# Kernel tuning notes

Hardware: AMD Instinct MI355X
Metric: run time of the kernel (lower is better)

Reference implementation:

```python
import jax, jax.numpy as jnp
import numpy as np
from jax import lax

N, CIN, P, CH, COUT = 1024, 3, 14, 256, 3
DN = ('NCHW', 'OIHW', 'NCHW')


def _conv(x, w, b, pad=1):
    y = lax.conv_general_dilated(x, w, (1, 1), [(pad, pad), (pad, pad)], dimension_numbers=DN)
    return y + b[None, :, None, None]


def _conv_transpose(x, w_t, b):
    # PyTorch ConvTranspose2d(k=3, stride=2, padding=1, output_padding=1):
    # equivalent to conv with lhs_dilation=2, padding (k-1-p, k-1-p+op) = (1, 2),
    # kernel with in/out swapped and spatially flipped. w_t: [in, out, 3, 3]
    w = jnp.flip(jnp.transpose(w_t, (1, 0, 2, 3)), axis=(2, 3))  # [out, in, 3, 3]
    y = lax.conv_general_dilated(x, w, (1, 1), [(1, 2), (1, 2)], lhs_dilation=(2, 2),
                                 dimension_numbers=DN)
    return y + b[None, :, None, None]


def setup_inputs() -> dict:
    key = jax.random.key(0)
    ks = jax.random.split(key, 16)
    s3 = lambda cin: 1.0 / np.sqrt(cin * 9)
    inp = {"x": jax.random.normal(ks[0], (N, CIN, P, P), dtype=jnp.float32)}
    inp["w1"] = jax.random.normal(ks[1], (CH, CIN, 3, 3), jnp.float32) * s3(CIN)
    inp["b1"] = jnp.zeros((CH,), jnp.float32)
    inp["w2"] = jax.random.normal(ks[2], (CH, CH, 3, 3), jnp.float32) * s3(CH)
    inp["b2"] = jnp.zeros((CH,), jnp.float32)
    inp["w3"] = jax.random.normal(ks[3], (CH, CH, 3, 3), jnp.float32) * s3(CH)
    inp["b3"] = jnp.zeros((CH,), jnp.float32)
    inp["w4"] = jax.random.normal(ks[4], (CH, CH, 3, 3), jnp.float32) * s3(CH)
    inp["b4"] = jnp.zeros((CH,), jnp.float32)
    inp["wt"] = jax.random.normal(ks[5], (CH, CH, 3, 3), jnp.float32) * s3(CH)  # [in, out, kh, kw]
    inp["bt"] = jnp.zeros((CH,), jnp.float32)
    inp["w5"] = jax.random.normal(ks[6], (COUT, CH, 1, 1), jnp.float32) * (1.0 / np.sqrt(CH))
    inp["b5"] = jnp.zeros((COUT,), jnp.float32)
    return inp


def reference(x, w1, b1, w2, b2, w3, b3, w4, b4, wt, bt, w5, b5):
    h = jax.nn.relu(_conv(x, w1, b1))
    h = jax.nn.relu(_conv(h, w2, b2))
    h = jax.nn.relu(_conv(h, w3, b3))
    h = jax.nn.relu(_conv(h, w4, b4))
    h = jax.nn.relu(_conv_transpose(h, wt, bt))  # [N, 256, 2P, 2P]
    h = _conv(h, w5, b5, pad=0)                   # 1x1 conv -> [N, 3, 2P, 2P]
    return jax.nn.sigmoid(h)
```

## Files before the change

### kernel.cpp

```cpp
#include <hip/hip_runtime.h>
#include <hip/hip_fp16.h>

typedef _Float16 half8 __attribute__((ext_vector_type(8)));
typedef _Float16 half4 __attribute__((ext_vector_type(4)));
typedef float floatx4 __attribute__((ext_vector_type(4)));

#define PLANE 65536
#define PK_ELEMS 589824

__global__ void repack_kernel(const float* __restrict__ w2, const float* __restrict__ w3,
                              const float* __restrict__ w4, const float* __restrict__ wt,
                              _Float16* __restrict__ pk) {
    int t = blockIdx.x * 256 + threadIdx.x;
    int l = t & 63;
    int idx = t >> 6;
    int nt = idx & 15; idx >>= 4;
    int ks = idx & 7;  idx >>= 3;
    int tap = idx % 9;
    int layer = idx / 9;
    int co = nt * 16 + (l & 15);
    int ci0 = ks * 32 + (l >> 4) * 8;
    const float* w = (layer == 0) ? w2 : (layer == 1) ? w3 : (layer == 2) ? w4 : wt;
    _Float16* dst = pk + (size_t)layer * PK_ELEMS + (((size_t)(tap * 8 + ks) * 16 + nt) * 64 + l) * 8;
    if (layer < 3) {
        for (int j = 0; j < 8; ++j)
            dst[j] = (_Float16)w[(co * 256 + (ci0 + j)) * 9 + tap];
    } else {
        int ky = tap / 3, kx = tap % 3;
        for (int j = 0; j < 8; ++j)
            dst[j] = (_Float16)w[((ci0 + j) * 256 + co) * 9 + (2 - ky) * 3 + (2 - kx)];
    }
}

__global__ __launch_bounds__(1024, 4) void conv1_kernel(const float* __restrict__ x,
                                                        const float* __restrict__ w1,
                                                        const float* __restrict__ b1,
                                                        _Float16* __restrict__ act) {
    __shared__ float inl[3][16][16];
    __shared__ float lw[256 * 27];
    __shared__ float lb1[256];
    int n = blockIdx.x, tid = threadIdx.x;
    if (tid < 768) ((float*)inl)[tid] = 0.f;
    __syncthreads();
    for (int i = tid; i < 3 * 196; i += 1024) {
        int ci = i / 196, r = i % 196, y = r / 14, xx = r % 14;
        inl[ci][y + 1][xx + 1] = x[(size_t)n * 588 + i];
    }
    for (int i = tid; i < 256 * 27; i += 1024) lw[i] = w1[i];
    if (tid < 256) lb1[tid] = b1[tid];
    __syncthreads();
    int p = tid >> 2, q = tid & 3;
    int py = p >> 4, px = p & 15;
    _Float16* ga = act + (size_t)n * PLANE + p * 256;
    int sw = (p & 7) << 3;
    if (py == 0 || py == 15 || px == 0 || px == 15) {
        for (int ci = 0; ci < 64; ++ci) { int co = q + ci * 4; ga[co ^ sw] = (_Float16)0.f; }
    } else {
        float vin[27];
        #pragma unroll
        for (int ci = 0; ci < 3; ++ci)
            #pragma unroll
            for (int ky = 0; ky < 3; ++ky)
                #pragma unroll
                for (int kx = 0; kx < 3; ++kx)
                    vin[ci * 9 + ky * 3 + kx] = inl[ci][py - 1 + ky][px - 1 + kx];
        for (int ci = 0; ci < 64; ++ci) {
            int co = q + ci * 4;
            float acc = lb1[co];
            const float* wp = &lw[co * 27];
            #pragma unroll
            for (int k = 0; k < 27; ++k) acc += vin[k] * wp[k];
            ga[co ^ sw] = (_Float16)fmaxf(acc, 0.f);
        }
    }
}


#define INIT_ACC(BIASPTR)                                                        \
    {                                                                            \
        _Pragma("unroll")                                                        \
        for (int ni = 0; ni < 4; ++ni) {                                         \
            floatx4 bv;                                                          \
            _Pragma("unroll")                                                    \
            for (int reg = 0; reg < 4; ++reg)                                    \
                bv[reg] = (BIASPTR)[(cg * 4 + ni) * 16 + kg * 4 + reg];          \
            _Pragma("unroll")                                                    \
            for (int i = 0; i < 7; ++i) acc[i][ni] = bv;                         \
        }                                                                        \
    }

#define BURST4(AF, BF)                                                           \
    {                                                                            \
        _Pragma("unroll")                                                        \
        for (int j = 0; j < 4; ++j) {                                            \
            acc[j][0] = __builtin_amdgcn_mfma_f32_16x16x32_f16(AF[0], BF[j], acc[j][0], 0, 0, 0); \
            acc[j][1] = __builtin_amdgcn_mfma_f32_16x16x32_f16(AF[1], BF[j], acc[j][1], 0, 0, 0); \
            acc[j][2] = __builtin_amdgcn_mfma_f32_16x16x32_f16(AF[2], BF[j], acc[j][2], 0, 0, 0); \
            acc[j][3] = __builtin_amdgcn_mfma_f32_16x16x32_f16(AF[3], BF[j], acc[j][3], 0, 0, 0); \
        }                                                                        \
    }

#define BURST3(AF, BF)                                                           \
    {                                                                            \
        _Pragma("unroll")                                                        \
        for (int j = 0; j < 3; ++j) {                                            \
            acc[4 + j][0] = __builtin_amdgcn_mfma_f32_16x16x32_f16(AF[0], BF[j], acc[4 + j][0], 0, 0, 0); \
            acc[4 + j][1] = __builtin_amdgcn_mfma_f32_16x16x32_f16(AF[1], BF[j], acc[4 + j][1], 0, 0, 0); \
            acc[4 + j][2] = __builtin_amdgcn_mfma_f32_16x16x32_f16(AF[2], BF[j], acc[4 + j][2], 0, 0, 0); \
            acc[4 + j][3] = __builtin_amdgcn_mfma_f32_16x16x32_f16(AF[3], BF[j], acc[4 + j][3], 0, 0, 0); \
        }                                                                        \
    }

#define LOAD_B4(BF, KS)                                                          \
    {                                                                            \
        int kk_ = ((KS) * 4 + kg) << 3;                                          \
        _Pragma("unroll")                                                        \
        for (int j = 0; j < 4; ++j)                                              \
            BF[j] = *(const half8*)(plane + poff_[j] + (kk_ ^ swj_[j]));         \
    }

#define LOAD_B3(BF, KS)                                                          \
    {                                                                            \
        int kk_ = ((KS) * 4 + kg) << 3;                                          \
        _Pragma("unroll")                                                        \
        for (int j = 0; j < 3; ++j)                                              \
            BF[j] = *(const half8*)(plane + poff_[4 + j] + (kk_ ^ swj_[4 + j])); \
    }

#define LOAD_A(AF, KS)                                                           \
    {                                                                            \
        _Pragma("unroll")                                                        \
        for (int ni = 0; ni < 4; ++ni)                                           \
            AF[ni] = *(const half8*)(pkt_ + (((KS) * 16 + cg * 4 + ni) * 64 + lane) * 8); \
    }

#define ACCUM_TAP(PKT, DOFF)                                                     \
    {                                                                            \
        const _Float16* pkt_ = (PKT);                                            \
        int poff_[7], swj_[7];                                                   \
        _Pragma("unroll")                                                        \
        for (int j = 0; j < 7; ++j) {                                            \
            poff_[j] = (pp[j] + (DOFF)) * 256;                                   \
            swj_[j] = (poff_[j] >> 5) & 56;                                      \
        }                                                                        \
        half8 aP[4], aN[4], bA[4], bB[3];                                        \
        LOAD_A(aP, 0)                                                            \
        LOAD_B4(bA, 0)                                                           \
        _Pragma("clang loop unroll(disable)")                                    \
        for (int ks2 = 0; ks2 < 4; ++ks2) {                                      \
            int e = ks2 * 2, o = e + 1;                                          \
            LOAD_B3(bB, e)                                                       \
            LOAD_A(aN, o)                                                        \
            BURST4(aP, bA)                                                       \
            LOAD_B4(bA, o)                                                       \
            BURST3(aP, bB)                                                       \
            LOAD_B3(bB, o)                                                       \
            if (ks2 < 3) LOAD_A(aP, e + 2)                                       \
            BURST4(aN, bA)                                                       \
            if (ks2 < 3) LOAD_B4(bA, e + 2)                                      \
            BURST3(aN, bB)                                                       \
        }                                                                        \
    }

#define EPILOGUE(RY, RX)                                                         \
    {                                                                            \
        _Pragma("unroll")                                                        \
        for (int i = 0; i < 7; ++i) {                                            \
            float s0 = 0.f, s1 = 0.f, s2 = 0.f;                                  \
            _Pragma("unroll")                                                    \
            for (int ni = 0; ni < 4; ++ni) {                                     \
                int co0 = (cg * 4 + ni) * 16 + kg * 4;                           \
                _Pragma("unroll")                                                \
                for (int reg = 0; reg < 4; ++reg) {                              \
                    float v = fmaxf(acc[i][ni][reg], 0.f);                       \
                    s0 += v * w5l[co0 + reg];                                    \
                    s1 += v * w5l[256 + co0 + reg];                              \
                    s2 += v * w5l[512 + co0 + reg];                              \
                }                                                                \
            }                                                                    \
            s0 += __shfl_xor(s0, 16, 64); s0 += __shfl_xor(s0, 32, 64);          \
            s1 += __shfl_xor(s1, 16, 64); s1 += __shfl_xor(s1, 32, 64);          \
            s2 += __shfl_xor(s2, 16, 64); s2 += __shfl_xor(s2, 32, 64);          \
            if (lane < 14) {                                                     \
                int pt_ = pg + 2 * i;                                            \
                int pix = (2 * pt_ + (RY)) * 28 + 2 * lane + (RX);               \
                atomicAdd(&o3[pix * 3 + 0], s0);                                 \
                atomicAdd(&o3[pix * 3 + 1], s1);                                 \
                atomicAdd(&o3[pix * 3 + 2], s2);                                 \
            }                                                                    \
        }                                                                        \
    }

__global__ __launch_bounds__(512, 2) void fused_kernel(const _Float16* __restrict__ act,
                                                       const _Float16* __restrict__ pk,
                                                       const float* __restrict__ b2,
                                                       const float* __restrict__ b3,
                                                       const float* __restrict__ b4,
                                                       const float* __restrict__ bt,
                                                       const float* __restrict__ w5,
                                                       const float* __restrict__ b5,
                                                       float* __restrict__ out) {
    __shared__ _Float16 plane[PLANE];
    __shared__ float o3[2352];
    __shared__ float w5l[768];
    int n = blockIdx.x, tid = threadIdx.x;
    const _Float16* ga = act + (size_t)n * PLANE;
    #pragma unroll
    for (int i = 0; i < 16; ++i)
        *(uint4*)(plane + (i * 512 + tid) * 8) = *(const uint4*)(ga + (i * 512 + tid) * 8);
    for (int i = tid; i < 2352; i += 512) o3[i] = b5[i % 3];
    for (int i = tid; i < 768; i += 512) w5l[i] = w5[i];

    int lane = tid & 63;
    int wid = __builtin_amdgcn_readfirstlane(tid >> 6);
    int cg = wid >> 1, pg = wid & 1;
    int col = lane & 15, kg = lane >> 4;

    int pp[7];
    {
        int xc = (col < 14) ? col : 13;
        #pragma unroll
        for (int i = 0; i < 7; ++i) pp[i] = (pg + 2 * i + 1) * 16 + xc + 1;
    }
    bool colok = (col < 14);
    __syncthreads();

    floatx4 acc[7][4];

    for (int L = 0; L < 3; ++L) {
        const _Float16* pkL = pk + (size_t)L * PK_ELEMS;
        const float* bias = (L == 0) ? b2 : (L == 1) ? b3 : b4;
        INIT_ACC(bias)
        for (int tap = 0; tap < 9; ++tap) {
            int doff = (tap / 3) * 16 + (tap % 3) - 17;
            ACCUM_TAP(pkL + (size_t)tap * 65536, doff)
        }
        __syncthreads();
        #pragma unroll
        for (int i = 0; i < 7; ++i) {
            int ppix = pp[i];
            int sw = (ppix & 7) << 3;
            if (colok) {
                #pragma unroll
                for (int ni = 0; ni < 4; ++ni) {
                    int co0 = (cg * 4 + ni) * 16 + kg * 4;
                    half4 h;
                    #pragma unroll
                    for (int reg = 0; reg < 4; ++reg) h[reg] = (_Float16)fmaxf(acc[i][ni][reg], 0.f);
                    *(half4*)(plane + ppix * 256 + (co0 ^ sw)) = h;
                }
            }
        }
        __syncthreads();
    }

    const _Float16* pkT = pk + (size_t)3 * PK_ELEMS;
    INIT_ACC(bt)
    ACCUM_TAP(pkT + 4 * 65536, 0)
    EPILOGUE(0, 0)
    INIT_ACC(bt)
    ACCUM_TAP(pkT + 3 * 65536, 0)
    ACCUM_TAP(pkT + 5 * 65536, 1)
    EPILOGUE(0, 1)
    INIT_ACC(bt)
    ACCUM_TAP(pkT + 1 * 65536, 0)
    ACCUM_TAP(pkT + 7 * 65536, 16)
    EPILOGUE(1, 0)
    INIT_ACC(bt)
    ACCUM_TAP(pkT + 0 * 65536, 0)
    ACCUM_TAP(pkT + 2 * 65536, 1)
    ACCUM_TAP(pkT + 6 * 65536, 16)
    ACCUM_TAP(pkT + 8 * 65536, 17)
    EPILOGUE(1, 1)

    __syncthreads();
    size_t ob = (size_t)n * 2352;
    for (int i = tid; i < 2352; i += 512) {
        int pix = i / 3, c = i % 3;
        float v = o3[i];
        out[ob + (size_t)c * 784 + pix] = 1.f / (1.f + __expf(-v));
    }
}

extern "C" void kernel_launch(void* const* d_in, const int* in_sizes, int n_in,
                              void* d_out, int out_size, void* d_ws, size_t ws_size,
                              hipStream_t stream) {
    const float* x  = (const float*)d_in[0];
    const float* w1 = (const float*)d_in[1];
    const float* b1 = (const float*)d_in[2];
    const float* w2 = (const float*)d_in[3];
    const float* b2 = (const float*)d_in[4];
    const float* w3 = (const float*)d_in[5];
    const float* b3 = (const float*)d_in[6];
    const float* w4 = (const float*)d_in[7];
    const float* b4 = (const float*)d_in[8];
    const float* wt = (const float*)d_in[9];
    const float* bt = (const float*)d_in[10];
    const float* w5 = (const float*)d_in[11];
    const float* b5 = (const float*)d_in[12];

    size_t need = ((size_t)1024 * PLANE + 4 * (size_t)PK_ELEMS) * sizeof(_Float16);
    if (ws_size < need) return;

    _Float16* act = (_Float16*)d_ws;
    _Float16* pk  = act + (size_t)1024 * PLANE;

    repack_kernel<<<1152, 256, 0, stream>>>(w2, w3, w4, wt, pk);
    conv1_kernel<<<1024, 1024, 0, stream>>>(x, w1, b1, act);
    fused_kernel<<<1024, 512, 0, stream>>>(act, pk, b2, b3, b4, bt, w5, b5, (float*)d_out);
}
```

Before: 889.8 us.

## Split fused conv work across 12 waves with 3 row groups and guard-padded LDS plane

Raises the fused kernel from 8 to 12 waves per block (768 threads), splitting rows into 3 groups so each wave holds 5 row tiles instead of 7. This cuts accumulator registers per wave and adds wave-level parallelism. Column mapping changes to use lanes 1..14 with zero guard regions around the LDS plane, so halo reads fall into zeroed memory. The cost is more redundant MFMA work on padding rows and columns, plus higher LDS usage per block.

```diff
diff --git a/kernel.cpp b/kernel.cpp
--- a/kernel.cpp
+++ b/kernel.cpp
@@ -7,6 +7,7 @@
 
 #define PLANE 65536
 #define PK_ELEMS 589824
+#define GUARD 4096
 
 __global__ void repack_kernel(const float* __restrict__ w2, const float* __restrict__ w3,
                               const float* __restrict__ w4, const float* __restrict__ wt,
@@ -85,14 +86,14 @@
             for (int reg = 0; reg < 4; ++reg)                                    \
                 bv[reg] = (BIASPTR)[(cg * 4 + ni) * 16 + kg * 4 + reg];          \
             _Pragma("unroll")                                                    \
-            for (int i = 0; i < 7; ++i) acc[i][ni] = bv;                         \
-        }                                                                        \
-    }
-
-#define BURST4(AF, BF)                                                           \
-    {                                                                            \
-        _Pragma("unroll")                                                        \
-        for (int j = 0; j < 4; ++j) {                                            \
+            for (int i = 0; i < 5; ++i) acc[i][ni] = bv;                         \
+        }                                                                        \
+    }
+
+#define BURST3(AF, BF)                                                           \
+    {                                                                            \
+        _Pragma("unroll")                                                        \
+        for (int j = 0; j < 3; ++j) {                                            \
             acc[j][0] = __builtin_amdgcn_mfma_f32_16x16x32_f16(AF[0], BF[j], acc[j][0], 0, 0, 0); \
             acc[j][1] = __builtin_amdgcn_mfma_f32_16x16x32_f16(AF[1], BF[j], acc[j][1], 0, 0, 0); \
             acc[j][2] = __builtin_amdgcn_mfma_f32_16x16x32_f16(AF[2], BF[j], acc[j][2], 0, 0, 0); \
@@ -100,31 +101,31 @@
         }                                                                        \
     }
 
-#define BURST3(AF, BF)                                                           \
-    {                                                                            \
-        _Pragma("unroll")                                                        \
-        for (int j = 0; j < 3; ++j) {                                            \
-            acc[4 + j][0] = __builtin_amdgcn_mfma_f32_16x16x32_f16(AF[0], BF[j], acc[4 + j][0], 0, 0, 0); \
-            acc[4 + j][1] = __builtin_amdgcn_mfma_f32_16x16x32_f16(AF[1], BF[j], acc[4 + j][1], 0, 0, 0); \
-            acc[4 + j][2] = __builtin_amdgcn_mfma_f32_16x16x32_f16(AF[2], BF[j], acc[4 + j][2], 0, 0, 0); \
-            acc[4 + j][3] = __builtin_amdgcn_mfma_f32_16x16x32_f16(AF[3], BF[j], acc[4 + j][3], 0, 0, 0); \
-        }                                                                        \
-    }
-
-#define LOAD_B4(BF, KS)                                                          \
+#define BURST2(AF, BF)                                                           \
+    {                                                                            \
+        _Pragma("unroll")                                                        \
+        for (int j = 0; j < 2; ++j) {                                            \
+            acc[3 + j][0] = __builtin_amdgcn_mfma_f32_16x16x32_f16(AF[0], BF[j], acc[3 + j][0], 0, 0, 0); \
+            acc[3 + j][1] = __builtin_amdgcn_mfma_f32_16x16x32_f16(AF[1], BF[j], acc[3 + j][1], 0, 0, 0); \
+            acc[3 + j][2] = __builtin_amdgcn_mfma_f32_16x16x32_f16(AF[2], BF[j], acc[3 + j][2], 0, 0, 0); \
+            acc[3 + j][3] = __builtin_amdgcn_mfma_f32_16x16x32_f16(AF[3], BF[j], acc[3 + j][3], 0, 0, 0); \
+        }                                                                        \
+    }
+
+#define LOAD_B3(BF, KS)                                                          \
     {                                                                            \
         int kk_ = ((KS) * 4 + kg) << 3;                                          \
         _Pragma("unroll")                                                        \
-        for (int j = 0; j < 4; ++j)                                              \
+        for (int j = 0; j < 3; ++j)                                              \
             BF[j] = *(const half8*)(plane + poff_[j] + (kk_ ^ swj_[j]));         \
     }
 
-#define LOAD_B3(BF, KS)                                                          \
+#define LOAD_B2(BF, KS)                                                          \
     {                                                                            \
         int kk_ = ((KS) * 4 + kg) << 3;                                          \
         _Pragma("unroll")                                                        \
-        for (int j = 0; j < 3; ++j)                                              \
-            BF[j] = *(const half8*)(plane + poff_[4 + j] + (kk_ ^ swj_[4 + j])); \
+        for (int j = 0; j < 2; ++j)                                              \
+            BF[j] = *(const half8*)(plane + poff_[3 + j] + (kk_ ^ swj_[3 + j])); \
     }
 
 #define LOAD_A(AF, KS)                                                           \
@@ -137,35 +138,35 @@
 #define ACCUM_TAP(PKT, DOFF)                                                     \
     {                                                                            \
         const _Float16* pkt_ = (PKT);                                            \
-        int poff_[7], swj_[7];                                                   \
-        _Pragma("unroll")                                                        \
-        for (int j = 0; j < 7; ++j) {                                            \
+        int poff_[5], swj_[5];                                                   \
+        _Pragma("unroll")                                                        \
+        for (int j = 0; j < 5; ++j) {                                            \
             poff_[j] = (pp[j] + (DOFF)) * 256;                                   \
             swj_[j] = (poff_[j] >> 5) & 56;                                      \
         }                                                                        \
-        half8 aP[4], aN[4], bA[4], bB[3];                                        \
+        half8 aP[4], aN[4], bA[3], bB[2];                                        \
         LOAD_A(aP, 0)                                                            \
-        LOAD_B4(bA, 0)                                                           \
+        LOAD_B3(bA, 0)                                                           \
         _Pragma("clang loop unroll(disable)")                                    \
         for (int ks2 = 0; ks2 < 4; ++ks2) {                                      \
             int e = ks2 * 2, o = e + 1;                                          \
-            LOAD_B3(bB, e)                                                       \
+            LOAD_B2(bB, e)                                                       \
             LOAD_A(aN, o)                                                        \
-            BURST4(aP, bA)                                                       \
-            LOAD_B4(bA, o)                                                       \
-            BURST3(aP, bB)                                                       \
-            LOAD_B3(bB, o)                                                       \
+            BURST3(aP, bA)                                                       \
+            LOAD_B3(bA, o)                                                       \
+            BURST2(aP, bB)                                                       \
+            LOAD_B2(bB, o)                                                       \
             if (ks2 < 3) LOAD_A(aP, e + 2)                                       \
-            BURST4(aN, bA)                                                       \
-            if (ks2 < 3) LOAD_B4(bA, e + 2)                                      \
-            BURST3(aN, bB)                                                       \
+            BURST3(aN, bA)                                                       \
+            if (ks2 < 3) LOAD_B3(bA, e + 2)                                      \
+            BURST2(aN, bB)                                                       \
         }                                                                        \
     }
 
 #define EPILOGUE(RY, RX)                                                         \
     {                                                                            \
         _Pragma("unroll")                                                        \
-        for (int i = 0; i < 7; ++i) {                                            \
+        for (int i = 0; i < 5; ++i) {                                            \
             float s0 = 0.f, s1 = 0.f, s2 = 0.f;                                  \
             _Pragma("unroll")                                                    \
             for (int ni = 0; ni < 4; ++ni) {                                     \
@@ -181,9 +182,9 @@
             s0 += __shfl_xor(s0, 16, 64); s0 += __shfl_xor(s0, 32, 64);          \
             s1 += __shfl_xor(s1, 16, 64); s1 += __shfl_xor(s1, 32, 64);          \
             s2 += __shfl_xor(s2, 16, 64); s2 += __shfl_xor(s2, 32, 64);          \
-            if (lane < 14) {                                                     \
-                int pt_ = pg + 2 * i;                                            \
-                int pix = (2 * pt_ + (RY)) * 28 + 2 * lane + (RX);               \
+            if ((i < 4 || t4) && lane < 16 && colok) {                           \
+                int yy = pg + 3 * i;                                             \
+                int pix = (2 * yy + (RY)) * 28 + 2 * (col - 1) + (RX);           \
                 atomicAdd(&o3[pix * 3 + 0], s0);                                 \
                 atomicAdd(&o3[pix * 3 + 1], s1);                                 \
                 atomicAdd(&o3[pix * 3 + 2], s2);                                 \
@@ -191,7 +192,7 @@
         }                                                                        \
     }
 
-__global__ __launch_bounds__(512, 2) void fused_kernel(const _Float16* __restrict__ act,
+__global__ __launch_bounds__(768, 3) void fused_kernel(const _Float16* __restrict__ act,
                                                        const _Float16* __restrict__ pk,
                                                        const float* __restrict__ b2,
                                                        const float* __restrict__ b3,
@@ -200,32 +201,36 @@
                                                        const float* __restrict__ w5,
                                                        const float* __restrict__ b5,
                                                        float* __restrict__ out) {
-    __shared__ _Float16 plane[PLANE];
+    __shared__ _Float16 plane[PLANE + 2 * GUARD];
     __shared__ float o3[2352];
     __shared__ float w5l[768];
     int n = blockIdx.x, tid = threadIdx.x;
     const _Float16* ga = act + (size_t)n * PLANE;
-    #pragma unroll
-    for (int i = 0; i < 16; ++i)
-        *(uint4*)(plane + (i * 512 + tid) * 8) = *(const uint4*)(ga + (i * 512 + tid) * 8);
-    for (int i = tid; i < 2352; i += 512) o3[i] = b5[i % 3];
-    for (int i = tid; i < 768; i += 512) w5l[i] = w5[i];
+    for (int i = tid; i < 1024; i += 768) {
+        int e = (i < 512) ? i : (i - 512) + (GUARD + PLANE) / 8;
+        *(uint4*)(plane + e * 8) = uint4{0, 0, 0, 0};
+    }
+    for (int i = tid; i < 8192; i += 768)
+        *(uint4*)(plane + GUARD + i * 8) = *(const uint4*)(ga + i * 8);
+    for (int i = tid; i < 2352; i += 768) o3[i] = b5[i % 3];
+    w5l[tid] = w5[tid];
 
     int lane = tid & 63;
     int wid = __builtin_amdgcn_readfirstlane(tid >> 6);
-    int cg = wid >> 1, pg = wid & 1;
+    int cg = wid & 3, pg = wid >> 2;
     int col = lane & 15, kg = lane >> 4;
-
-    int pp[7];
-    {
-        int xc = (col < 14) ? col : 13;
-        #pragma unroll
-        for (int i = 0; i < 7; ++i) pp[i] = (pg + 2 * i + 1) * 16 + xc + 1;
-    }
-    bool colok = (col < 14);
+    bool colok = (col >= 1 && col <= 14);
+    bool t4 = (pg < 2);
+
+    int pp[5];
+    #pragma unroll
+    for (int i = 0; i < 5; ++i) {
+        int rr = pg + 3 * i + 1; if (rr > 14) rr = 13;
+        pp[i] = rr * 16 + col + 16;
+    }
     __syncthreads();
 
-    floatx4 acc[7][4];
+    floatx4 acc[5][4];
 
     for (int L = 0; L < 3; ++L) {
         const _Float16* pkL = pk + (size_t)L * PK_ELEMS;
@@ -237,10 +242,10 @@
         }
         __syncthreads();
         #pragma unroll
-        for (int i = 0; i < 7; ++i) {
-            int ppix = pp[i];
-            int sw = (ppix & 7) << 3;
-            if (colok) {
+        for (int i = 0; i < 5; ++i) {
+            if ((i < 4 || t4) && colok) {
+                int ppix = pp[i];
+                int sw = (ppix & 7) << 3;
                 #pragma unroll
                 for (int ni = 0; ni < 4; ++ni) {
                     int co0 = (cg * 4 + ni) * 16 + kg * 4;
@@ -275,7 +280,7 @@
 
     __syncthreads();
     size_t ob = (size_t)n * 2352;
-    for (int i = tid; i < 2352; i += 512) {
+    for (int i = tid; i < 2352; i += 768) {
         int pix = i / 3, c = i % 3;
         float v = o3[i];
         out[ob + (size_t)c * 784 + pix] = 1.f / (1.f + __expf(-v));
@@ -307,5 +312,5 @@
 
     repack_kernel<<<1152, 256, 0, stream>>>(w2, w3, w4, wt, pk);
     conv1_kernel<<<1024, 1024, 0, stream>>>(x, w1, b1, act);
-    fused_kernel<<<1024, 512, 0, stream>>>(act, pk, b2, b3, b4, bt, w5, b5, (float*)d_out);
+    fused_kernel<<<1024, 768, 0, stream>>>(act, pk, b2, b3, b4, bt, w5, b5, (float*)d_out);
 }
```

New measurement: 1.051 ms. 18.1% more time.
